# Kernel optimization log

Hardware: AMD Instinct MI355X
Metric: run time of the kernel (lower is better)

## Reference

```python
import jax, jax.numpy as jnp
import numpy as np

B, S, D = 2, 2048, 2048
H, HKV = 32, 8
HD = D // H  # 64
NEG_INF = -1e9


def _rope_tables(seq_len, head_dim):
    inv_freq = 1.0 / (10000.0 ** (np.arange(0, head_dim, 2, dtype=np.float32) / head_dim))
    t = np.arange(seq_len, dtype=np.float32)
    freqs = np.outer(t, inv_freq)                      # (S, HD/2)
    emb = np.concatenate([freqs, freqs], axis=-1)      # (S, HD)
    cos = np.cos(emb)[None, None]                      # (1,1,S,HD)
    sin = np.sin(emb)[None, None]
    return jnp.asarray(cos), jnp.asarray(sin)


def setup_inputs() -> dict:
    key = jax.random.key(0)
    ks = jax.random.split(key, 5)
    hidden_states = jax.random.normal(ks[0], (B, S, D), dtype=jnp.float32)
    # causal additive mask: 0 where allowed, -inf (large negative) where masked
    causal = jnp.tril(jnp.ones((S, S), dtype=jnp.bool_))
    attention_mask = jnp.where(causal, 0.0, NEG_INF).astype(jnp.float32)
    attention_mask = jnp.broadcast_to(attention_mask[None, None], (B, 1, S, S))
    cos, sin = _rope_tables(S, HD)
    sc = 0.02
    Wq = jax.random.normal(ks[1], (D, H * HD), dtype=jnp.float32) * sc
    Wk = jax.random.normal(ks[2], (D, HKV * HD), dtype=jnp.float32) * sc
    Wv = jax.random.normal(ks[3], (D, HKV * HD), dtype=jnp.float32) * sc
    Wo = jax.random.normal(ks[4], (H * HD, D), dtype=jnp.float32) * sc
    return {"hidden_states": hidden_states, "attention_mask": attention_mask,
            "cos": cos, "sin": sin, "Wq": Wq, "Wk": Wk, "Wv": Wv, "Wo": Wo}


def _rotate_half(x):
    x1, x2 = jnp.split(x, 2, axis=-1)
    return jnp.concatenate([-x2, x1], axis=-1)


def _apply_rope(x, cos, sin):
    # x: (B, h, S, HD); cos/sin: (1,1,S,HD)
    return x * cos + _rotate_half(x) * sin


def reference(hidden_states, attention_mask, cos, sin, Wq, Wk, Wv, Wo):
    b, s, _ = hidden_states.shape
    scale = 1.0 / np.sqrt(HD)
    q = (hidden_states @ Wq).reshape(b, s, H, HD).transpose(0, 2, 1, 3)    # (B,H,S,HD)
    k = (hidden_states @ Wk).reshape(b, s, HKV, HD).transpose(0, 2, 1, 3)  # (B,HKV,S,HD)
    v = (hidden_states @ Wv).reshape(b, s, HKV, HD).transpose(0, 2, 1, 3)
    q = _apply_rope(q, cos, sin)
    k = _apply_rope(k, cos, sin)
    # GQA: group query heads per kv head without materializing repeated KV
    g = H // HKV
    qg = q.reshape(b, HKV, g, s, HD)
    scores = jnp.einsum('bkgqd,bksd->bkgqs', qg, k) * scale               # (B,HKV,g,S,S)
    scores = scores + attention_mask[:, :, None]                          # broadcast (B,1,1,S,S)
    attn = jax.nn.softmax(scores, axis=-1)
    out = jnp.einsum('bkgqs,bksd->bkgqd', attn, v)                        # (B,HKV,g,S,HD)
    out = out.reshape(b, H, s, HD).transpose(0, 2, 1, 3).reshape(b, s, H * HD)
    return out @ Wo
```

## Files before the change

### kernel.cpp

```cpp
#include <hip/hip_runtime.h>
#include <math.h>

typedef _Float16 half8 __attribute__((ext_vector_type(8)));
typedef _Float16 half4 __attribute__((ext_vector_type(4)));
typedef _Float16 half2 __attribute__((ext_vector_type(2)));
typedef float f32x4 __attribute__((ext_vector_type(4)));

#define S_LEN 2048
#define DM    2048
#define NH    32
#define NKV   8

#define QSCALE 0.1803368801111204f
#define NSHIFT -11.541560327111707f

#if __has_builtin(__builtin_amdgcn_exp2f)
#define EXP2(x) __builtin_amdgcn_exp2f(x)
#else
#define EXP2(x) __builtin_exp2f(x)
#endif

__device__ __forceinline__ half2 pkrtz(float a, float b) {
    return __builtin_bit_cast(half2, __builtin_amdgcn_cvt_pkrtz(a, b));
}

__device__ __forceinline__ void async16(const void* g, void* l) {
    __builtin_amdgcn_global_load_lds(
        (const __attribute__((address_space(1))) unsigned int*)g,
        (__attribute__((address_space(3))) unsigned int*)l, 16, 0, 0);
}

__global__ __launch_bounds__(256) void cast_h(const float* __restrict__ x,
                                              _Float16* __restrict__ y, int n)
{
    int i = (blockIdx.x * 256 + threadIdx.x) * 4;
    if (i >= n) return;
    float4 v = *(const float4*)(x + i);
    half4 o = {(_Float16)v.x, (_Float16)v.y, (_Float16)v.z, (_Float16)v.w};
    *(half4*)(y + i) = o;
}

__global__ __launch_bounds__(256) void transpose_all(
    const float* __restrict__ Wq, const float* __restrict__ Wk,
    const float* __restrict__ Wv, const float* __restrict__ Wo,
    _Float16* __restrict__ Wqkv_t, _Float16* __restrict__ Wo_t)
{
    const int z = blockIdx.z;
    const float* W; _Float16* Wt; int N;
    if (z == 0)      { W = Wq; Wt = Wqkv_t;                        N = 2048; }
    else if (z == 1) { W = Wk; Wt = Wqkv_t + (size_t)2048 * 2048;  N = 512;  }
    else if (z == 2) { W = Wv; Wt = Wqkv_t + (size_t)2560 * 2048;  N = 512;  }
    else             { W = Wo; Wt = Wo_t;                          N = 2048; }
    if ((int)blockIdx.x * 32 >= N) return;

    __shared__ float t[32][33];
    const int n0 = blockIdx.x * 32, k0 = blockIdx.y * 32;
    const int tx = threadIdx.x & 31, ty = threadIdx.x >> 5;
#pragma unroll
    for (int i = 0; i < 32; i += 8)
        t[ty + i][tx] = W[(size_t)(k0 + ty + i) * N + n0 + tx];
    __syncthreads();
#pragma unroll
    for (int i = 0; i < 32; i += 8)
        Wt[(size_t)(n0 + ty + i) * 2048 + k0 + tx] = (_Float16)t[tx][ty + i];
}

__global__ __launch_bounds__(256) void gemm_h(
    const _Float16* __restrict__ A, const _Float16* __restrict__ Bt,
    void* __restrict__ Cout, int N, int K, int mode,
    const float* __restrict__ cosT, const float* __restrict__ sinT)
{
    __shared__ __align__(16) _Float16 Al[128 * 32];
    __shared__ __align__(16) _Float16 Bl[128 * 32];
    const int tid = threadIdx.x;
    const int bm = blockIdx.y * 128, bn = blockIdx.x * 128;
    const int wave = tid >> 6, lane = tid & 63;
    const int wm = (wave & 1) * 64, wn = (wave >> 1) * 64;
    const int lm = lane & 15, quad = lane >> 4;

    const int f0 = tid * 16, f1 = 4096 + tid * 16;
    const int r0 = f0 >> 6, r1 = f1 >> 6;
    const int c0 = ((f0 >> 4) & 3) ^ (r0 & 3);
    const int c1 = ((f1 >> 4) & 3) ^ (r1 & 3);

    f32x4 acc[4][4];
#pragma unroll
    for (int i = 0; i < 4; ++i)
#pragma unroll
        for (int j = 0; j < 4; ++j) acc[i][j] = (f32x4){0.f, 0.f, 0.f, 0.f};

    for (int k0 = 0; k0 < K; k0 += 32) {
        async16(A + (size_t)(bm + r0) * K + k0 + c0 * 8, (char*)Al + f0);
        async16(A + (size_t)(bm + r1) * K + k0 + c1 * 8, (char*)Al + f1);
        async16(Bt + (size_t)(bn + r0) * K + k0 + c0 * 8, (char*)Bl + f0);
        async16(Bt + (size_t)(bn + r1) * K + k0 + c1 * 8, (char*)Bl + f1);
        __syncthreads();
        half8 af[4], bf[4];
#pragma unroll
        for (int i = 0; i < 4; ++i) {
            int row = wm + i * 16 + lm;
            af[i] = *(const half8*)(Al + row * 32 + ((quad ^ (row & 3)) << 3));
        }
#pragma unroll
        for (int j = 0; j < 4; ++j) {
            int row = wn + j * 16 + lm;
            bf[j] = *(const half8*)(Bl + row * 32 + ((quad ^ (row & 3)) << 3));
        }
#pragma unroll
        for (int i = 0; i < 4; ++i)
#pragma unroll
            for (int j = 0; j < 4; ++j)
                acc[i][j] = __builtin_amdgcn_mfma_f32_16x16x32_f16(af[i], bf[j], acc[i][j], 0, 0, 0);
        __syncthreads();
    }

    const int mrow = bm + wm + quad * 4;
    if (mode == 0) {
        float* C = (float*)Cout;
        const int col0 = bn + wn + lm;
#pragma unroll
        for (int i = 0; i < 4; ++i)
#pragma unroll
            for (int r = 0; r < 4; ++r) {
                int m = mrow + i * 16 + r;
#pragma unroll
                for (int j = 0; j < 4; ++j)
                    C[(size_t)m * N + col0 + j * 16] = acc[i][j][r];
            }
        return;
    }

    _Float16* Cq = (_Float16*)Cout;
    _Float16* Ck = Cq + (size_t)2 * NH * S_LEN * 64;
    _Float16* Cv = Ck + (size_t)2 * NKV * S_LEN * 64;
    const int colbase = bn + wn;
    const int region = (colbase >= 2560) ? 2 : (colbase >= 2048) ? 1 : 0;

    if (region == 2) {
        const int head = (colbase - 2560) >> 6;
#pragma unroll
        for (int i = 0; i < 4; ++i)
#pragma unroll
            for (int r = 0; r < 4; ++r) {
                int m = mrow + i * 16 + r;
                int b = m >> 11, s = m & 2047;
#pragma unroll
                for (int j = 0; j < 4; ++j)
                    Cv[((((size_t)b * NKV + head) << 6) + lm + j * 16) * S_LEN + s] =
                        (_Float16)acc[i][j][r];
            }
        return;
    }

    const float qscale = (region == 0) ? QSCALE : 1.0f;
    const int head = (region == 0) ? (colbase >> 6) : ((colbase - 2048) >> 6);
    _Float16* Cdst = (region == 0) ? Cq : Ck;
    const int nh = (region == 0) ? NH : NKV;
#pragma unroll
    for (int i = 0; i < 4; ++i)
#pragma unroll
        for (int r = 0; r < 4; ++r) {
            int m = mrow + i * 16 + r;
            int b = m >> 11, s = m & 2047;
            const float* cp = cosT + s * 64 + lm;
            const float* sp = sinT + s * 64 + lm;
            float a0 = acc[i][0][r], a1 = acc[i][1][r], a2 = acc[i][2][r], a3 = acc[i][3][r];
            float o0 = (a0 * cp[0]  - a2 * sp[0])  * qscale;
            float o1 = (a1 * cp[16] - a3 * sp[16]) * qscale;
            float o2 = (a2 * cp[32] + a0 * sp[32]) * qscale;
            float o3 = (a3 * cp[48] + a1 * sp[48]) * qscale;
            _Float16* d = Cdst + ((((size_t)b * nh + head) * S_LEN + s) << 6) + lm;
            d[0]  = (_Float16)o0;
            d[16] = (_Float16)o1;
            d[32] = (_Float16)o2;
            d[48] = (_Float16)o3;
        }
}

#define LSWOFS(row, halfofs) \
    ((row) * 64 + (((((halfofs) >> 3) & 7) ^ ((row) & 7)) << 3) + ((halfofs) & 7))

__global__ __launch_bounds__(256, 2) void attn_h(
    const _Float16* __restrict__ q, const _Float16* __restrict__ k,
    const _Float16* __restrict__ vt, _Float16* __restrict__ x2)
{
    __shared__ __align__(16) _Float16 Ks[64 * 64];
    __shared__ __align__(16) _Float16 Vts[64 * 64];

    const int kvh = blockIdx.y, b = blockIdx.z;
    const int tid = threadIdx.x;
    const int wave = tid >> 6, lane = tid & 63;
    const int lm = lane & 15, quad = lane >> 4;
    const int h = kvh * 4 + wave;

    const int qtT[2] = {63 - (int)blockIdx.x, (int)blockIdx.x};
    const int ktm[2] = {(qtT[0] * 32 + 31) >> 6, (qtT[1] * 32 + 31) >> 6};

    const _Float16* kbase  = k  + ((((size_t)b * NKV + kvh) * S_LEN) << 6);
    const _Float16* vtbase = vt + ((((size_t)b * NKV + kvh) << 6) * S_LEN);

    half8 qf[2][2][2];
#pragma unroll
    for (int tp = 0; tp < 2; ++tp) {
        const _Float16* qb = q + ((((size_t)b * NH + h) * S_LEN + qtT[tp] * 32) << 6);
#pragma unroll
        for (int i = 0; i < 2; ++i)
#pragma unroll
            for (int kk = 0; kk < 2; ++kk)
                qf[tp][i][kk] = *(const half8*)(qb + (i * 16 + lm) * 64 + kk * 32 + quad * 8);
    }

    f32x4 accOT[2][2][4];
    float lpart[2][2];
#pragma unroll
    for (int tp = 0; tp < 2; ++tp)
#pragma unroll
        for (int i = 0; i < 2; ++i) {
            lpart[tp][i] = 0.f;
#pragma unroll
            for (int j = 0; j < 4; ++j) accOT[tp][i][j] = (f32x4){0.f, 0.f, 0.f, 0.f};
        }

    const int f0 = tid * 16, f1 = 4096 + tid * 16;
    const int r0 = f0 >> 7, r1 = f1 >> 7;
    const int c0 = ((f0 >> 4) & 7) ^ (r0 & 7);
    const int c1 = ((f1 >> 4) & 7) ^ (r1 & 7);

    for (int kt = 0; kt <= ktm[0]; ++kt) {
        async16((const char*)kbase + (size_t)kt * 8192 + r0 * 128 + c0 * 16, (char*)Ks + f0);
        async16((const char*)kbase + (size_t)kt * 8192 + r1 * 128 + c1 * 16, (char*)Ks + f1);
        async16((const char*)vtbase + (size_t)r0 * 4096 + kt * 128 + c0 * 16, (char*)Vts + f0);
        async16((const char*)vtbase + (size_t)r1 * 4096 + kt * 128 + c1 * 16, (char*)Vts + f1);
        __syncthreads();

        half8 kf[4][2];
        half4 vtf[4][4];
#pragma unroll
        for (int t = 0; t < 4; ++t) {
#pragma unroll
            for (int kk = 0; kk < 2; ++kk)
                kf[t][kk] = *(const half8*)(Ks + LSWOFS(t * 16 + lm, kk * 32 + quad * 8));
#pragma unroll
            for (int j = 0; j < 4; ++j)
                vtf[j][t] = *(const half4*)(Vts + LSWOFS(j * 16 + lm, t * 16 + quad * 4));
        }

#pragma unroll
        for (int tp = 0; tp < 2; ++tp) {
            if (kt > ktm[tp]) continue;
            const bool diag = (kt == ktm[tp]);
#pragma unroll
            for (int i = 0; i < 2; ++i) {
                f32x4 sc[4];
#pragma unroll
                for (int t = 0; t < 4; ++t) {
                    f32x4 z = (f32x4){NSHIFT, NSHIFT, NSHIFT, NSHIFT};
                    z = __builtin_amdgcn_mfma_f32_16x16x32_f16(kf[t][0], qf[tp][i][0], z, 0, 0, 0);
                    z = __builtin_amdgcn_mfma_f32_16x16x32_f16(kf[t][1], qf[tp][i][1], z, 0, 0, 0);
                    sc[t] = z;
                }
                if (diag) {
                    const int qpos = qtT[tp] * 32 + i * 16 + lm;
#pragma unroll
                    for (int t = 0; t < 4; ++t)
#pragma unroll
                        for (int r = 0; r < 4; ++r) {
                            int key = kt * 64 + t * 16 + quad * 4 + r;
                            if (key > qpos) sc[t][r] = -30000.f;
                        }
                }
                half4 pt[4];
                float lp = 0.f;
#pragma unroll
                for (int t = 0; t < 4; ++t) {
                    float p0 = EXP2(sc[t][0]), p1 = EXP2(sc[t][1]);
                    float p2 = EXP2(sc[t][2]), p3 = EXP2(sc[t][3]);
                    lp += (p0 + p1) + (p2 + p3);
                    half2 lo = pkrtz(p0, p1);
                    half2 hi = pkrtz(p2, p3);
                    pt[t] = (half4){lo[0], lo[1], hi[0], hi[1]};
                }
                lpart[tp][i] += lp;
#pragma unroll
                for (int j = 0; j < 4; ++j)
#pragma unroll
                    for (int t = 0; t < 4; ++t)
                        accOT[tp][i][j] = __builtin_amdgcn_mfma_f32_16x16x16f16(
                            vtf[j][t], pt[t], accOT[tp][i][j], 0, 0, 0);
            }
        }
        __syncthreads();
    }

#pragma unroll
    for (int tp = 0; tp < 2; ++tp)
#pragma unroll
        for (int i = 0; i < 2; ++i) {
            float l = lpart[tp][i];
            l += __shfl_xor(l, 16);
            l += __shfl_xor(l, 32);
            const float inv = 1.f / l;
            const size_t row = (size_t)b * S_LEN + qtT[tp] * 32 + i * 16 + lm;
#pragma unroll
            for (int j = 0; j < 4; ++j) {
                f32x4 o = accOT[tp][i][j];
                half2 lo = pkrtz(o[0] * inv, o[1] * inv);
                half2 hi = pkrtz(o[2] * inv, o[3] * inv);
                half4 ov = {lo[0], lo[1], hi[0], hi[1]};
                *(half4*)(x2 + row * DM + h * 64 + j * 16 + quad * 4) = ov;
            }
        }
}

extern "C" void kernel_launch(void* const* d_in, const int* in_sizes, int n_in,
                              void* d_out, int out_size, void* d_ws, size_t ws_size,
                              hipStream_t stream)
{
    const float* hidden = (const float*)d_in[0];
    const float* cosT = (const float*)d_in[2];
    const float* sinT = (const float*)d_in[3];
    const float* Wq = (const float*)d_in[4];
    const float* Wk = (const float*)d_in[5];
    const float* Wv = (const float*)d_in[6];
    const float* Wo = (const float*)d_in[7];
    float* out = (float*)d_out;

    _Float16* w = (_Float16*)d_ws;
    _Float16* hid_h  = w;  w += (size_t)4096 * 2048;
    _Float16* Wqkv_t = w;  w += (size_t)3072 * 2048;
    _Float16* Wo_t   = w;  w += (size_t)2048 * 2048;
    _Float16* qh     = w;  w += (size_t)2 * NH * S_LEN * 64;
    _Float16* kh     = w;  w += (size_t)2 * NKV * S_LEN * 64;
    _Float16* vth    = w;  w += (size_t)2 * NKV * S_LEN * 64;
    _Float16* x2h    = w;

    dim3 blk(256);
    cast_h<<<dim3(8192), blk, 0, stream>>>(hidden, hid_h, 8388608);
    transpose_all<<<dim3(64, 64, 4), blk, 0, stream>>>(Wq, Wk, Wv, Wo, Wqkv_t, Wo_t);

    gemm_h<<<dim3(24, 32), blk, 0, stream>>>(hid_h, Wqkv_t, qh, 3072, 2048, 1, cosT, sinT);

    attn_h<<<dim3(32, 8, 2), blk, 0, stream>>>(qh, kh, vth, x2h);

    gemm_h<<<dim3(16, 32), blk, 0, stream>>>(x2h, Wo_t, out, 2048, 2048, 0, nullptr, nullptr);
}
```

Baseline: 341.4 us.

## Double GEMM K-tile to 64 and vectorize transposed V stores

The fp16 MFMA GEMM now stages a 64-wide K slice per iteration, using an 8-way XOR swizzle in LDS, and runs two MFMA sub-steps per load. This halves the number of barrier pairs and loop iterations so more math is issued per synchronization. The V-region epilogue also packs four consecutive sequence positions into one half4 store instead of four scalar stores, using round-toward-zero conversion. LDS use doubles to 32 KB per block, which may reduce occupancy.

```diff
diff --git a/kernel.cpp b/kernel.cpp
--- a/kernel.cpp
+++ b/kernel.cpp
@@ -65,23 +65,29 @@
         Wt[(size_t)(n0 + ty + i) * 2048 + k0 + tx] = (_Float16)t[tx][ty + i];
 }
 
+#define LSW64(basep, row, halfofs) \
+    (*(const half8*)((basep) + (row) * 64 + (((((halfofs) >> 3) & 7) ^ ((row) & 7)) << 3)))
+
 __global__ __launch_bounds__(256) void gemm_h(
     const _Float16* __restrict__ A, const _Float16* __restrict__ Bt,
     void* __restrict__ Cout, int N, int K, int mode,
     const float* __restrict__ cosT, const float* __restrict__ sinT)
 {
-    __shared__ __align__(16) _Float16 Al[128 * 32];
-    __shared__ __align__(16) _Float16 Bl[128 * 32];
+    __shared__ __align__(16) _Float16 Al[128 * 64];
+    __shared__ __align__(16) _Float16 Bl[128 * 64];
     const int tid = threadIdx.x;
     const int bm = blockIdx.y * 128, bn = blockIdx.x * 128;
     const int wave = tid >> 6, lane = tid & 63;
     const int wm = (wave & 1) * 64, wn = (wave >> 1) * 64;
     const int lm = lane & 15, quad = lane >> 4;
 
-    const int f0 = tid * 16, f1 = 4096 + tid * 16;
-    const int r0 = f0 >> 6, r1 = f1 >> 6;
-    const int c0 = ((f0 >> 4) & 3) ^ (r0 & 3);
-    const int c1 = ((f1 >> 4) & 3) ^ (r1 & 3);
+    int ro[4], co[4];
+#pragma unroll
+    for (int u = 0; u < 4; ++u) {
+        const int f = u * 4096 + tid * 16;
+        ro[u] = f >> 7;
+        co[u] = ((f >> 4) & 7) ^ (ro[u] & 7);
+    }
 
     f32x4 acc[4][4];
 #pragma unroll
@@ -89,28 +95,30 @@
 #pragma unroll
         for (int j = 0; j < 4; ++j) acc[i][j] = (f32x4){0.f, 0.f, 0.f, 0.f};
 
-    for (int k0 = 0; k0 < K; k0 += 32) {
-        async16(A + (size_t)(bm + r0) * K + k0 + c0 * 8, (char*)Al + f0);
-        async16(A + (size_t)(bm + r1) * K + k0 + c1 * 8, (char*)Al + f1);
-        async16(Bt + (size_t)(bn + r0) * K + k0 + c0 * 8, (char*)Bl + f0);
-        async16(Bt + (size_t)(bn + r1) * K + k0 + c1 * 8, (char*)Bl + f1);
+    for (int k0 = 0; k0 < K; k0 += 64) {
+#pragma unroll
+        for (int u = 0; u < 4; ++u) {
+            async16(A + (size_t)(bm + ro[u]) * K + k0 + co[u] * 8,
+                    (char*)Al + u * 4096 + tid * 16);
+            async16(Bt + (size_t)(bn + ro[u]) * K + k0 + co[u] * 8,
+                    (char*)Bl + u * 4096 + tid * 16);
+        }
         __syncthreads();
-        half8 af[4], bf[4];
-#pragma unroll
-        for (int i = 0; i < 4; ++i) {
-            int row = wm + i * 16 + lm;
-            af[i] = *(const half8*)(Al + row * 32 + ((quad ^ (row & 3)) << 3));
-        }
-#pragma unroll
-        for (int j = 0; j < 4; ++j) {
-            int row = wn + j * 16 + lm;
-            bf[j] = *(const half8*)(Bl + row * 32 + ((quad ^ (row & 3)) << 3));
-        }
-#pragma unroll
-        for (int i = 0; i < 4; ++i)
+#pragma unroll
+        for (int kp = 0; kp < 2; ++kp) {
+            half8 af[4], bf[4];
+#pragma unroll
+            for (int i = 0; i < 4; ++i)
+                af[i] = LSW64(Al, wm + i * 16 + lm, kp * 32 + quad * 8);
 #pragma unroll
             for (int j = 0; j < 4; ++j)
-                acc[i][j] = __builtin_amdgcn_mfma_f32_16x16x32_f16(af[i], bf[j], acc[i][j], 0, 0, 0);
+                bf[j] = LSW64(Bl, wn + j * 16 + lm, kp * 32 + quad * 8);
+#pragma unroll
+            for (int i = 0; i < 4; ++i)
+#pragma unroll
+                for (int j = 0; j < 4; ++j)
+                    acc[i][j] = __builtin_amdgcn_mfma_f32_16x16x32_f16(af[i], bf[j], acc[i][j], 0, 0, 0);
+        }
         __syncthreads();
     }
 
@@ -139,16 +147,17 @@
     if (region == 2) {
         const int head = (colbase - 2560) >> 6;
 #pragma unroll
-        for (int i = 0; i < 4; ++i)
-#pragma unroll
-            for (int r = 0; r < 4; ++r) {
-                int m = mrow + i * 16 + r;
-                int b = m >> 11, s = m & 2047;
-#pragma unroll
-                for (int j = 0; j < 4; ++j)
-                    Cv[((((size_t)b * NKV + head) << 6) + lm + j * 16) * S_LEN + s] =
-                        (_Float16)acc[i][j][r];
+        for (int i = 0; i < 4; ++i) {
+            const int m0 = mrow + i * 16;
+            const int b = m0 >> 11, s0 = m0 & 2047;
+#pragma unroll
+            for (int j = 0; j < 4; ++j) {
+                half2 lo = pkrtz(acc[i][j][0], acc[i][j][1]);
+                half2 hi = pkrtz(acc[i][j][2], acc[i][j][3]);
+                half4 ov = {lo[0], lo[1], hi[0], hi[1]};
+                *(half4*)(Cv + ((((size_t)b * NKV + head) << 6) + lm + j * 16) * S_LEN + s0) = ov;
             }
+        }
         return;
     }
 
```

Measured after the change: 339.5 us. No clear change (-0.5%).
